# Performance work log

Hardware: AMD Instinct MI355X
Metric: run time of the kernel (lower is better)

The kernel has to match this reference:

```python
import jax, jax.numpy as jnp
import numpy as np

ITEMS_TOTAL = 50000
DIM = 64
BATCH = 16
N_PER_GRAPH = 50


def setup_inputs() -> dict:
    key = jax.random.key(0)
    k1, k2, k3, k4 = jax.random.split(key, 4)
    nodes = jax.random.randint(k1, (BATCH * N_PER_GRAPH,), 0, ITEMS_TOTAL, dtype=jnp.int64)
    nodes_output = jax.random.normal(k2, (BATCH * N_PER_GRAPH, DIM), dtype=jnp.float32)
    emb_table = jax.random.normal(k3, (ITEMS_TOTAL, DIM), dtype=jnp.float32)
    alpha = jax.random.uniform(k4, (ITEMS_TOTAL, 1), dtype=jnp.float32)  # torch.rand init
    return {"nodes": nodes, "nodes_output": nodes_output, "emb_table": emb_table,
            "alpha": alpha, "n_per_graph": N_PER_GRAPH}


def reference(nodes, nodes_output, emb_table, alpha, n_per_graph):
    items_total, dim = emb_table.shape
    n = int(n_per_graph)
    b = nodes.shape[0] // n
    idx_b = nodes.reshape(b, n)            # (B, n) item indices per graph
    feat_b = nodes_output.reshape(b, n, dim)  # (B, n, F)

    def per_graph(idx, feat):
        # beta: 1 for items present in this graph, 0 otherwise
        beta = jnp.zeros((items_total, 1), dtype=emb_table.dtype).at[idx].set(1.0)
        # gate the full table: untouched rows keep emb, touched rows scaled by (1-alpha)
        embed = (1.0 - beta * alpha) * emb_table          # (items_total, F)
        updated = embed[idx] + alpha[idx] * feat          # (n, F)
        return embed.at[idx].set(updated)

    return jax.vmap(per_graph)(idx_b, feat_b)             # (B, items_total, F)
```

## Files before the change

### kernel.cpp

```cpp
#include <hip/hip_runtime.h>
#include <hip/hip_bf16.h>


#define DIM 64
#define SEGS (DIM / 4)
#define BLOCK 256
#define RPB 32

template <int CB>
__global__ __launch_bounds__(BLOCK) void ggu_kernel(
    const int* __restrict__ nodes,
    const float4* __restrict__ feat,
    const float4* __restrict__ emb,
    const float* __restrict__ alpha,
    float4* __restrict__ out,
    int items, int n, int Brt)
{
    const int B = (CB > 0) ? CB : Brt;
    const int row0 = blockIdx.x * RPB;

    extern __shared__ unsigned int smem[];
    unsigned int* rowmask = smem;
    int* sidx = (int*)(smem + RPB);

    const int total = B * n;
    if (threadIdx.x < RPB) rowmask[threadIdx.x] = 0u;
    __syncthreads();
    for (int t = threadIdx.x; t < total; t += BLOCK) {
        int id = nodes[t];
        sidx[t] = id;
        int local = id - row0;
        if ((unsigned)local < (unsigned)RPB)
            atomicOr(&rowmask[local], 1u << (t / n));
    }
    __syncthreads();

    const int seg  = threadIdx.x & (SEGS - 1);
    const int rloc = threadIdx.x >> 4;
    const int r0 = row0 + rloc;
    const int r1 = r0 + 16;
    const bool ok0 = r0 < items;
    const bool ok1 = r1 < items;

    float4 e0 = ok0 ? emb[(size_t)r0 * SEGS + seg] : float4{0, 0, 0, 0};
    float4 e1 = ok1 ? emb[(size_t)r1 * SEGS + seg] : float4{0, 0, 0, 0};
    const unsigned int m0 = ok0 ? rowmask[rloc] : 0u;
    const unsigned int m1 = ok1 ? rowmask[rloc + 16] : 0u;

    const size_t bstride = (size_t)items * SEGS;
    float4* po0 = out + (size_t)r0 * SEGS + seg;
    float4* po1 = out + (size_t)r1 * SEGS + seg;

    if ((m0 | m1) == 0u) {
        if (CB > 0) {
            #pragma unroll
            for (int b = 0; b < CB; ++b) {
                if (ok0) po0[b * bstride] = e0;
                if (ok1) po1[b * bstride] = e1;
            }
        } else {
            for (int b = 0; b < B; ++b) {
                if (ok0) po0[b * bstride] = e0;
                if (ok1) po1[b * bstride] = e1;
            }
        }
    } else {
        const float a0 = ok0 ? alpha[r0] : 0.0f;
        const float a1 = ok1 ? alpha[r1] : 0.0f;
        for (int b = 0; b < B; ++b) {
            float4 v0 = e0, v1 = e1;
            if ((m0 >> b) & 1u) {
                int jl = 0;
                #pragma unroll 1
                for (int j = 0; j < n; ++j)
                    if (sidx[b * n + j] == r0) jl = j;
                const float4 f = feat[(size_t)(b * n + jl) * SEGS + seg];
                const float om = 1.0f - a0;
                v0.x = om * e0.x + a0 * f.x; v0.y = om * e0.y + a0 * f.y;
                v0.z = om * e0.z + a0 * f.z; v0.w = om * e0.w + a0 * f.w;
            }
            if ((m1 >> b) & 1u) {
                int jl = 0;
                #pragma unroll 1
                for (int j = 0; j < n; ++j)
                    if (sidx[b * n + j] == r1) jl = j;
                const float4 f = feat[(size_t)(b * n + jl) * SEGS + seg];
                const float om = 1.0f - a1;
                v1.x = om * e1.x + a1 * f.x; v1.y = om * e1.y + a1 * f.y;
                v1.z = om * e1.z + a1 * f.z; v1.w = om * e1.w + a1 * f.w;
            }
            if (ok0) po0[b * bstride] = v0;
            if (ok1) po1[b * bstride] = v1;
        }
    }
}

extern "C" void kernel_launch(void* const* d_in, const int* in_sizes, int n_in,
                              void* d_out, int out_size, void* d_ws, size_t ws_size,
                              hipStream_t stream) {
    const int*   nodes = (const int*)d_in[0];
    const float* feat  = (const float*)d_in[1];
    const float* emb   = (const float*)d_in[2];
    const float* alpha = (const float*)d_in[3];

    const int items = in_sizes[3];
    const int B     = out_size / (items * DIM);
    const int n     = in_sizes[0] / B;

    const int grid = (items + RPB - 1) / RPB;
    const size_t lds_bytes = (size_t)(RPB + B * n) * sizeof(unsigned int);

    if (B == 16) {
        ggu_kernel<16><<<grid, BLOCK, lds_bytes, stream>>>(
            nodes, (const float4*)feat, (const float4*)emb, alpha,
            (float4*)d_out, items, n, B);
    } else {
        ggu_kernel<0><<<grid, BLOCK, lds_bytes, stream>>>(
            nodes, (const float4*)feat, (const float4*)emb, alpha,
            (float4*)d_out, items, n, B);
    }
}
```

Measured before the change: 214.9 us.

## Parallelize over batch in grid and use per-graph last-index table via atomicMax

New measurement: 235.4 us. +9.6%, slower.

```diff
diff --git a/kernel.cpp b/kernel.cpp
--- a/kernel.cpp
+++ b/kernel.cpp
@@ -1,96 +1,56 @@
 #include <hip/hip_runtime.h>
-#include <hip/hip_bf16.h>
 
 
 #define DIM 64
 #define SEGS (DIM / 4)
 #define BLOCK 256
-#define RPB 32
+#define KF 5
+#define TILE (BLOCK * KF)
+#define NROWS (TILE / SEGS)
 
-template <int CB>
-__global__ __launch_bounds__(BLOCK) void ggu_kernel(
+__global__ __launch_bounds__(BLOCK) void ggu_stream(
     const int* __restrict__ nodes,
     const float4* __restrict__ feat,
     const float4* __restrict__ emb,
     const float* __restrict__ alpha,
     float4* __restrict__ out,
-    int items, int n, int Brt)
+    int items, int n)
 {
-    const int B = (CB > 0) ? CB : Brt;
-    const int row0 = blockIdx.x * RPB;
+    const int b = blockIdx.y;
+    const size_t rowsF4 = (size_t)items * SEGS;
+    const size_t base   = (size_t)blockIdx.x * TILE;
+    const int row0      = (int)(base / SEGS);
 
-    extern __shared__ unsigned int smem[];
-    unsigned int* rowmask = smem;
-    int* sidx = (int*)(smem + RPB);
-
-    const int total = B * n;
-    if (threadIdx.x < RPB) rowmask[threadIdx.x] = 0u;
+    __shared__ int lastj[NROWS];
+    for (int i = threadIdx.x; i < NROWS; i += BLOCK) lastj[i] = -1;
     __syncthreads();
-    for (int t = threadIdx.x; t < total; t += BLOCK) {
-        int id = nodes[t];
-        sidx[t] = id;
-        int local = id - row0;
-        if ((unsigned)local < (unsigned)RPB)
-            atomicOr(&rowmask[local], 1u << (t / n));
+    for (int j = threadIdx.x; j < n; j += BLOCK) {
+        const int local = nodes[b * n + j] - row0;
+        if ((unsigned)local < (unsigned)NROWS)
+            atomicMax(&lastj[local], j);
     }
     __syncthreads();
 
-    const int seg  = threadIdx.x & (SEGS - 1);
-    const int rloc = threadIdx.x >> 4;
-    const int r0 = row0 + rloc;
-    const int r1 = r0 + 16;
-    const bool ok0 = r0 < items;
-    const bool ok1 = r1 < items;
+    const float4* e = emb + base;
+    float4* o = out + (size_t)b * rowsF4 + base;
 
-    float4 e0 = ok0 ? emb[(size_t)r0 * SEGS + seg] : float4{0, 0, 0, 0};
-    float4 e1 = ok1 ? emb[(size_t)r1 * SEGS + seg] : float4{0, 0, 0, 0};
-    const unsigned int m0 = ok0 ? rowmask[rloc] : 0u;
-    const unsigned int m1 = ok1 ? rowmask[rloc + 16] : 0u;
-
-    const size_t bstride = (size_t)items * SEGS;
-    float4* po0 = out + (size_t)r0 * SEGS + seg;
-    float4* po1 = out + (size_t)r1 * SEGS + seg;
-
-    if ((m0 | m1) == 0u) {
-        if (CB > 0) {
-            #pragma unroll
-            for (int b = 0; b < CB; ++b) {
-                if (ok0) po0[b * bstride] = e0;
-                if (ok1) po1[b * bstride] = e1;
+    #pragma unroll
+    for (int k = 0; k < KF; ++k) {
+        const int off = k * BLOCK + (int)threadIdx.x;
+        if (base + (size_t)off < rowsF4) {
+            float4 v = e[off];
+            const int jl = lastj[off >> 4];
+            if (jl >= 0) {
+                const int row = row0 + (off >> 4);
+                const float a = alpha[row];
+                const float4 f = feat[(size_t)(b * n + jl) * SEGS + (off & (SEGS - 1))];
+                const float om = 1.0f - a;
+                v.x = om * v.x + a * f.x;
+                v.y = om * v.y + a * f.y;
+                v.z = om * v.z + a * f.z;
+                v.w = om * v.w + a * f.w;
             }
-        } else {
-            for (int b = 0; b < B; ++b) {
-                if (ok0) po0[b * bstride] = e0;
-                if (ok1) po1[b * bstride] = e1;
-            }
-        }
-    } else {
-        const float a0 = ok0 ? alpha[r0] : 0.0f;
-        const float a1 = ok1 ? alpha[r1] : 0.0f;
-        for (int b = 0; b < B; ++b) {
-            float4 v0 = e0, v1 = e1;
-            if ((m0 >> b) & 1u) {
-                int jl = 0;
-                #pragma unroll 1
-                for (int j = 0; j < n; ++j)
-                    if (sidx[b * n + j] == r0) jl = j;
-                const float4 f = feat[(size_t)(b * n + jl) * SEGS + seg];
-                const float om = 1.0f - a0;
-                v0.x = om * e0.x + a0 * f.x; v0.y = om * e0.y + a0 * f.y;
-                v0.z = om * e0.z + a0 * f.z; v0.w = om * e0.w + a0 * f.w;
-            }
-            if ((m1 >> b) & 1u) {
-                int jl = 0;
-                #pragma unroll 1
-                for (int j = 0; j < n; ++j)
-                    if (sidx[b * n + j] == r1) jl = j;
-                const float4 f = feat[(size_t)(b * n + jl) * SEGS + seg];
-                const float om = 1.0f - a1;
-                v1.x = om * e1.x + a1 * f.x; v1.y = om * e1.y + a1 * f.y;
-                v1.z = om * e1.z + a1 * f.z; v1.w = om * e1.w + a1 * f.w;
-            }
-            if (ok0) po0[b * bstride] = v0;
-            if (ok1) po1[b * bstride] = v1;
+            o[off] = v;
         }
     }
 }
@@ -107,16 +67,11 @@
     const int B     = out_size / (items * DIM);
     const int n     = in_sizes[0] / B;
 
-    const int grid = (items + RPB - 1) / RPB;
-    const size_t lds_bytes = (size_t)(RPB + B * n) * sizeof(unsigned int);
+    const size_t rowsF4 = (size_t)items * SEGS;
+    const unsigned gx = (unsigned)((rowsF4 + TILE - 1) / TILE);
+    dim3 grid(gx, (unsigned)B);
 
-    if (B == 16) {
-        ggu_kernel<16><<<grid, BLOCK, lds_bytes, stream>>>(
-            nodes, (const float4*)feat, (const float4*)emb, alpha,
-            (float4*)d_out, items, n, B);
-    } else {
-        ggu_kernel<0><<<grid, BLOCK, lds_bytes, stream>>>(
-            nodes, (const float4*)feat, (const float4*)emb, alpha,
-            (float4*)d_out, items, n, B);
-    }
+    ggu_stream<<<grid, BLOCK, 0, stream>>>(
+        nodes, (const float4*)feat, (const float4*)emb, alpha,
+        (float4*)d_out, items, n);
 }
```
